# Performance work log

Hardware: AMD Instinct MI355X
Metric: run time of the kernel (lower is better)

Reference implementation:

```python
import jax, jax.numpy as jnp
import numpy as np

D_MODEL = 1024
NUM_HEADS = 16


def setup_inputs() -> dict:
    key = jax.random.key(0)
    ks = jax.random.split(key, 5)
    sigma = (2.0 / (D_MODEL + D_MODEL)) ** 0.5
    def trunc(k):
        # truncated normal in [-3*sigma, 3*sigma], std sigma
        return sigma * jax.random.truncated_normal(k, -3.0, 3.0, (D_MODEL, D_MODEL), jnp.float32)
    x = jax.random.normal(ks[0], (4, 2048, D_MODEL), jnp.float32)
    return {
        "x": x,
        "W_Q": trunc(ks[1]),
        "W_K": trunc(ks[2]),
        "W_V": trunc(ks[3]),
        "W_O": trunc(ks[4]),
    }


def _mha(x, W_Q, W_K, W_V, W_O):
    B, S, D = x.shape
    H = NUM_HEADS
    dk = D // H
    # Linear stores W as (d_out, d_in); einsum '... d_in, d_out d_in -> ... d_out'
    Q = jnp.einsum('bsd,ed->bse', x, W_Q).reshape(B, S, H, dk).transpose(0, 2, 1, 3)
    K = jnp.einsum('bsd,ed->bse', x, W_K).reshape(B, S, H, dk).transpose(0, 2, 1, 3)
    V = jnp.einsum('bsd,ed->bse', x, W_V).reshape(B, S, H, dk).transpose(0, 2, 1, 3)
    scores = jnp.einsum('bhnd,bhmd->bhnm', Q, K) / jnp.sqrt(jnp.asarray(dk, x.dtype))
    causal = jnp.tril(jnp.ones((S, S), bool))
    scores = jnp.where(causal, scores, -jnp.inf)
    attn = jax.nn.softmax(scores, axis=-1)
    out = jnp.einsum('bhnm,bhmd->bhnd', attn, V)  # [B,H,S,dk]
    out = out.transpose(0, 2, 1, 3).reshape(B, S, D)
    return jnp.einsum('bsd,ed->bse', out, W_O)


def reference(x, W_Q, W_K, W_V, W_O):
    return _mha(x, W_Q, W_K, W_V, W_O)
```

## Files before the change

kernel.cpp:

```cpp
#include <hip/hip_runtime.h>
#include <hip/hip_bf16.h>
#include <stdint.h>


typedef unsigned short u16;
typedef short bf16x8 __attribute__((ext_vector_type(8)));
typedef float f32x4 __attribute__((ext_vector_type(4)));
typedef unsigned short u16x8 __attribute__((ext_vector_type(8)));

#define S_LEN 2048
#define DMODEL 1024
#define NH 16

__device__ __forceinline__ u16 f2bf(float f) {
    unsigned u = __builtin_bit_cast(unsigned, f);
    unsigned r = (u + 0x7fffu + ((u >> 16) & 1u)) >> 16;
    return (u16)r;
}

__device__ __forceinline__ float fast_exp2(float x) {
    return __builtin_amdgcn_exp2f(x);
}

__device__ __forceinline__ unsigned cvtpk_bf16(float lo, float hi_) {
    unsigned r;
    asm("v_cvt_pk_bf16_f32 %0, %1, %2" : "=v"(r) : "v"(lo), "v"(hi_));
    return r;
}

__device__ __forceinline__ void gll16(const void* g, void* s) {
    __builtin_amdgcn_global_load_lds((const __attribute__((address_space(1))) unsigned*)g,
                                     (__attribute__((address_space(3))) unsigned*)s, 16, 0, 0);
}

__global__ __launch_bounds__(256) void cast_all(
    const float* __restrict__ x, const float* __restrict__ wq, const float* __restrict__ wk,
    const float* __restrict__ wv, const float* __restrict__ wo,
    u16* __restrict__ xb, u16* __restrict__ wqkv, u16* __restrict__ wob, int nx) {
    const int NW = DMODEL * DMODEL;
    int i4 = (blockIdx.x * 256 + threadIdx.x) * 4;
    const float* src; u16* dst; int off;
    if (i4 < nx)             { src = x;  dst = xb;            off = i4; }
    else if (i4 < nx + NW)   { src = wq; dst = wqkv;          off = i4 - nx; }
    else if (i4 < nx + 2*NW) { src = wk; dst = wqkv + NW;     off = i4 - nx - NW; }
    else if (i4 < nx + 3*NW) { src = wv; dst = wqkv + 2*NW;   off = i4 - nx - 2*NW; }
    else                     { src = wo; dst = wob;           off = i4 - nx - 3*NW; }
    float4 v = *reinterpret_cast<const float4*>(src + off);
    ushort4 o4; o4.x = f2bf(v.x); o4.y = f2bf(v.y); o4.z = f2bf(v.z); o4.w = f2bf(v.w);
    *reinterpret_cast<ushort4*>(dst + off) = o4;
}

template <typename OUT>
__global__ __launch_bounds__(256) void gemm_bt(const u16* __restrict__ A, const u16* __restrict__ B,
                                               OUT* __restrict__ C, int M, int N, int K,
                                               int qcols, float qscale, u16* __restrict__ vt) {
    __shared__ u16 As[128 * 64];
    __shared__ u16 Bs[128 * 64];
    __shared__ u16 Ts[4][16 * 72];
    const int m0 = blockIdx.y * 128, n0 = blockIdx.x * 128;
    const int t = threadIdx.x, w = t >> 6, l = t & 63;
    const int hi = l >> 4;
    const int wr = w >> 1, wc = w & 1;
    f32x4 acc[4][4] = {};

    const int lr = l >> 3;
    const int lc = l & 7;
    const int gcol = (lc ^ lr) * 8;
    const u16* Ag = A + (size_t)(m0 + w * 32 + lr) * K + gcol;
    const u16* Bg = B + (size_t)(n0 + w * 32 + lr) * K + gcol;

    for (int k0 = 0; k0 < K; k0 += 64) {
        __syncthreads();
#pragma unroll
        for (int c = 0; c < 4; c++) {
            gll16(Ag + (size_t)c * 8 * K + k0, As + w * 2048 + c * 512);
            gll16(Bg + (size_t)c * 8 * K + k0, Bs + w * 2048 + c * 512);
        }
        __syncthreads();
#pragma unroll
        for (int kk = 0; kk < 2; kk++) {
            bf16x8 af[4], bfr[4];
#pragma unroll
            for (int mi = 0; mi < 4; mi++)
                af[mi] = *(const bf16x8*)&As[(wr * 64 + mi * 16 + (l & 15)) * 64 +
                                             (((kk * 4 + hi) ^ (l & 7)) * 8)];
#pragma unroll
            for (int ni = 0; ni < 4; ni++)
                bfr[ni] = *(const bf16x8*)&Bs[(wc * 64 + ni * 16 + (l & 15)) * 64 +
                                              (((kk * 4 + hi) ^ (l & 7)) * 8)];
#pragma unroll
            for (int mi = 0; mi < 4; mi++)
#pragma unroll
                for (int ni = 0; ni < 4; ni++)
                    acc[mi][ni] = __builtin_amdgcn_mfma_f32_16x16x32_bf16(af[mi], bfr[ni], acc[mi][ni], 0, 0, 0);
        }
    }

    if (vt != nullptr && n0 >= 2048) {
        const int mw = m0 + wr * 64;
        const int bq = mw >> 11;
        const int s0w = mw & (S_LEN - 1);
        const int hd = ((n0 + wc * 64) - 2048) >> 6;
        u16* tb = &Ts[w][0];
#pragma unroll
        for (int ni = 0; ni < 4; ni++) {
#pragma unroll
            for (int mi = 0; mi < 4; mi++) {
                uint2 pk = make_uint2(cvtpk_bf16(acc[mi][ni][0], acc[mi][ni][1]),
                                      cvtpk_bf16(acc[mi][ni][2], acc[mi][ni][3]));
                *(uint2*)&tb[(l & 15) * 72 + mi * 16 + hi * 4] = pk;
            }
            bf16x8 r0 = *(const bf16x8*)&tb[(l & 15) * 72 + hi * 16];
            bf16x8 r1 = *(const bf16x8*)&tb[(l & 15) * 72 + hi * 16 + 8];
            size_t vrow = ((size_t)(bq * 16 + hd) * 64 + ni * 16 + (l & 15)) * S_LEN + s0w + hi * 16;
            *(u16x8*)&vt[vrow]     = (u16x8)r0;
            *(u16x8*)&vt[vrow + 8] = (u16x8)r1;
        }
    } else {
#pragma unroll
        for (int mi = 0; mi < 4; mi++)
#pragma unroll
            for (int ni = 0; ni < 4; ni++)
#pragma unroll
                for (int j = 0; j < 4; j++) {
                    int r = m0 + wr * 64 + mi * 16 + hi * 4 + j;
                    int c = n0 + wc * 64 + ni * 16 + (l & 15);
                    float v = acc[mi][ni][j];
                    if (c < qcols) v *= qscale;
                    if constexpr (__is_same(OUT, u16)) C[(size_t)r * N + c] = f2bf(v);
                    else                               C[(size_t)r * N + c] = v;
                }
    }
}

__global__ __launch_bounds__(512, 4) void attn(const u16* __restrict__ QKV, const u16* __restrict__ VT,
                                               u16* __restrict__ O) {
    const int bh = blockIdx.x, p = blockIdx.y;
    const int b = bh >> 4, h = bh & 15;
    const int t = threadIdx.x, w = t >> 6, l = t & 63;
    const int q = l & 15, hi = l >> 4, s7 = q & 7;

    __shared__ u16 SM[2][2][64][64];
    __shared__ u16 PS[8][16][64];

    const int srow = t >> 3, sblk = t & 7;
    const int gs = (sblk ^ (srow & 7)) * 8;
    const u16* Kg = QKV + (size_t)(b * S_LEN + srow) * 3072 + 1024 + h * 64 + gs;
    const u16* Vg = VT + (size_t)(bh * 64 + srow) * S_LEN + gs;

    const int kA0 = q * 128 + ((hi ^ s7) << 4);
    const int kA1 = kA0 ^ 64;
    const char* smbase = (const char*)&SM[0][0][0][0];

    char* pbase = (char*)&PS[w][0][0];
    const int pw0 = q * 128 + ((((0 * 2) + (hi >> 1)) ^ s7) << 4) + ((hi & 1) << 3);
    const int pw1 = q * 128 + ((((1 * 2) + (hi >> 1)) ^ s7) << 4) + ((hi & 1) << 3);
    const int pw2 = q * 128 + ((((2 * 2) + (hi >> 1)) ^ s7) << 4) + ((hi & 1) << 3);
    const int pw3 = q * 128 + ((((3 * 2) + (hi >> 1)) ^ s7) << 4) + ((hi & 1) << 3);
    const int pr0 = q * 128 + (((0 * 4 + hi) ^ s7) << 4);
    const int pr1 = q * 128 + (((1 * 4 + hi) ^ s7) << 4);

#pragma unroll 1
    for (int part = 0; part < 2; ++part) {
        const int q128 = (part == 0 ? p : 15 - p) * 128;
        const int nt = q128 / 64 + 2;
        const int qglob = q128 + w * 16 + q;

        bf16x8 qf[2];
#pragma unroll
        for (int kk = 0; kk < 2; kk++)
            qf[kk] = *(const bf16x8*)&QKV[(size_t)(b * S_LEN + qglob) * 3072 + h * 64 + kk * 32 + hi * 8];

        f32x4 oacc[4] = {};
        float ss0 = 0.f, ss1 = 0.f;

        gll16(Kg, (u16*)&SM[0][0][0][0] + t * 8);
        gll16(Vg, (u16*)&SM[0][1][0][0] + t * 8);
        __syncthreads();

        const u16* KgT = Kg + (size_t)64 * 3072;
        const u16* VgT = Vg + 64;

#pragma unroll 1
        for (int tt = 0; tt < nt; ++tt) {
            const int cur = tt & 1;
            if (tt + 1 < nt) {
                gll16(KgT, (u16*)&SM[cur ^ 1][0][0][0] + t * 8);
                gll16(VgT, (u16*)&SM[cur ^ 1][1][0][0] + t * 8);
                KgT += (size_t)64 * 3072;
                VgT += 64;
            }
            const int kv0 = tt * 64;
            if (q128 + w * 16 + 15 >= kv0) {
                const char* kb = smbase + cur * 16384;
                f32x4 sacc[4] = {};
                __builtin_amdgcn_s_setprio(1);
#pragma unroll
                for (int kk = 0; kk < 2; kk++) {
                    const char* ka = kb + (kk ? kA1 : kA0);
#pragma unroll
                    for (int ni = 0; ni < 4; ni++) {
                        bf16x8 kf = *(const bf16x8*)(ka + ni * 2048);
                        sacc[ni] = __builtin_amdgcn_mfma_f32_16x16x32_bf16(kf, qf[kk], sacc[ni], 0, 0, 0);
                    }
                }
                __builtin_amdgcn_s_setprio(0);
                const int r0 = qglob - kv0;
                if (r0 < 63) {
                    const int rth = r0 - hi * 4;
#pragma unroll
                    for (int ni = 0; ni < 4; ni++)
#pragma unroll
                        for (int j = 0; j < 4; j++)
                            if (ni * 16 + j > rth) sacc[ni][j] = -1e30f;
                }
                float pv[4][4];
#pragma unroll
                for (int ni = 0; ni < 4; ni++)
#pragma unroll
                    for (int j = 0; j < 4; j++) pv[ni][j] = fast_exp2(sacc[ni][j] - 8.0f);
                ss0 += ((pv[0][0] + pv[0][1]) + (pv[0][2] + pv[0][3]))
                     + ((pv[1][0] + pv[1][1]) + (pv[1][2] + pv[1][3]));
                ss1 += ((pv[2][0] + pv[2][1]) + (pv[2][2] + pv[2][3]))
                     + ((pv[3][0] + pv[3][1]) + (pv[3][2] + pv[3][3]));
                *(uint2*)(pbase + pw0) = make_uint2(cvtpk_bf16(pv[0][0], pv[0][1]), cvtpk_bf16(pv[0][2], pv[0][3]));
                *(uint2*)(pbase + pw1) = make_uint2(cvtpk_bf16(pv[1][0], pv[1][1]), cvtpk_bf16(pv[1][2], pv[1][3]));
                *(uint2*)(pbase + pw2) = make_uint2(cvtpk_bf16(pv[2][0], pv[2][1]), cvtpk_bf16(pv[2][2], pv[2][3]));
                *(uint2*)(pbase + pw3) = make_uint2(cvtpk_bf16(pv[3][0], pv[3][1]), cvtpk_bf16(pv[3][2], pv[3][3]));
                bf16x8 pf0 = *(const bf16x8*)(pbase + pr0);
                bf16x8 pf1 = *(const bf16x8*)(pbase + pr1);
                const char* vb = kb + 8192;
                __builtin_amdgcn_s_setprio(1);
#pragma unroll
                for (int kk = 0; kk < 2; kk++) {
                    const char* va = vb + (kk ? kA1 : kA0);
                    bf16x8 pf = kk ? pf1 : pf0;
#pragma unroll
                    for (int di = 0; di < 4; di++) {
                        bf16x8 vf = *(const bf16x8*)(va + di * 2048);
                        oacc[di] = __builtin_amdgcn_mfma_f32_16x16x32_bf16(vf, pf, oacc[di], 0, 0, 0);
                    }
                }
                __builtin_amdgcn_s_setprio(0);
            }
            __syncthreads();
        }

        float ssr = ss0 + ss1;
        ssr += __shfl_xor(ssr, 16, 64);
        ssr += __shfl_xor(ssr, 32, 64);
        float inv = 1.0f / ssr;
#pragma unroll
        for (int di = 0; di < 4; di++) {
            ushort4 o4;
            o4.x = f2bf(oacc[di][0] * inv);
            o4.y = f2bf(oacc[di][1] * inv);
            o4.z = f2bf(oacc[di][2] * inv);
            o4.w = f2bf(oacc[di][3] * inv);
            *(ushort4*)&O[(size_t)(b * S_LEN + qglob) * DMODEL + h * 64 + di * 16 + hi * 4] = o4;
        }
    }
}

extern "C" void kernel_launch(void* const* d_in, const int* in_sizes, int n_in,
                              void* d_out, int out_size, void* d_ws, size_t ws_size,
                              hipStream_t stream) {
    const float* x  = (const float*)d_in[0];
    const float* wq = (const float*)d_in[1];
    const float* wk = (const float*)d_in[2];
    const float* wv = (const float*)d_in[3];
    const float* wo = (const float*)d_in[4];
    const int nx = in_sizes[0];
    const int BS = nx / DMODEL;
    const int NW = DMODEL * DMODEL;

    u16* xb   = (u16*)d_ws;
    u16* wqkv = xb + (size_t)nx;
    u16* wob  = wqkv + (size_t)3 * NW;
    u16* qkv  = wob + (size_t)NW;
    u16* vt   = qkv + (size_t)BS * 3072;
    u16* ob   = vt + (size_t)nx;

    int ncast = (nx + 4 * NW) / 4 / 256;
    cast_all<<<ncast, 256, 0, stream>>>(x, wq, wk, wv, wo, xb, wqkv, wob, nx);

    const float QSC = 0.125f * 1.44269504088896f;
    gemm_bt<u16><<<dim3(3072 / 128, BS / 128), 256, 0, stream>>>(xb, wqkv, qkv, BS, 3072, DMODEL,
                                                                 DMODEL, QSC, vt);

    attn<<<dim3((BS / S_LEN) * NH, 8), 512, 0, stream>>>(qkv, vt, ob);

    gemm_bt<float><<<dim3(DMODEL / 128, BS / 128), 256, 0, stream>>>(ob, wob, (float*)d_out, BS, DMODEL, DMODEL,
                                                                     0, 1.0f, nullptr);
}
```

Baseline: 159.4 us.

## Fuse both causal query parts into one KV sweep sharing K/V tiles

The attention kernel used to stream K/V tiles twice per block, once for each of its two paired query chunks (p and 15-p). It now holds both chunks' Q fragments and accumulators and walks the KV sequence once, reusing each staged K/V tile and its LDS fragment reads for both chunks. This cuts global loads and barriers for the shorter chunk. In exchange it doubles accumulator and Q register use, which may lower occupancy under launch_bounds(512,4), and it adds a second P scratch buffer in LDS.

Result: slower. 186.6 us (+17.1%).

```diff
diff --git a/kernel.cpp b/kernel.cpp
--- a/kernel.cpp
+++ b/kernel.cpp
@@ -141,7 +141,7 @@
     const int q = l & 15, hi = l >> 4, s7 = q & 7;
 
     __shared__ u16 SM[2][2][64][64];
-    __shared__ u16 PS[8][16][64];
+    __shared__ u16 PS[8][2][16][64];
 
     const int srow = t >> 3, sblk = t & 7;
     const int gs = (sblk ^ (srow & 7)) * 8;
@@ -152,7 +152,8 @@
     const int kA1 = kA0 ^ 64;
     const char* smbase = (const char*)&SM[0][0][0][0];
 
-    char* pbase = (char*)&PS[w][0][0];
+    char* pb0 = (char*)&PS[w][0][0][0];
+    char* pb1 = (char*)&PS[w][1][0][0];
     const int pw0 = q * 128 + ((((0 * 2) + (hi >> 1)) ^ s7) << 4) + ((hi & 1) << 3);
     const int pw1 = q * 128 + ((((1 * 2) + (hi >> 1)) ^ s7) << 4) + ((hi & 1) << 3);
     const int pw2 = q * 128 + ((((2 * 2) + (hi >> 1)) ^ s7) << 4) + ((hi & 1) << 3);
@@ -160,104 +161,148 @@
     const int pr0 = q * 128 + (((0 * 4 + hi) ^ s7) << 4);
     const int pr1 = q * 128 + (((1 * 4 + hi) ^ s7) << 4);
 
+    const int part1 = 15 - p;
+    const int q128_0 = p * 128, q128_1 = part1 * 128;
+    const int nt0 = 2 * p + 2, nt1 = 2 * part1 + 2;
+    const int qglob0 = q128_0 + w * 16 + q;
+    const int qglob1 = q128_1 + w * 16 + q;
+
+    bf16x8 qf0[2], qf1[2];
+#pragma unroll
+    for (int kk = 0; kk < 2; kk++) {
+        qf0[kk] = *(const bf16x8*)&QKV[(size_t)(b * S_LEN + qglob0) * 3072 + h * 64 + kk * 32 + hi * 8];
+        qf1[kk] = *(const bf16x8*)&QKV[(size_t)(b * S_LEN + qglob1) * 3072 + h * 64 + kk * 32 + hi * 8];
+    }
+
+    f32x4 oacc0[4] = {}, oacc1[4] = {};
+    float ssA = 0.f, ssB = 0.f;
+
+    gll16(Kg, (u16*)&SM[0][0][0][0] + t * 8);
+    gll16(Vg, (u16*)&SM[0][1][0][0] + t * 8);
+    __syncthreads();
+
+    const u16* KgT = Kg + (size_t)64 * 3072;
+    const u16* VgT = Vg + 64;
+
+    auto softmax_part = [&](f32x4* sacc, int qglob, int kv0, char* pb, float& ss,
+                            bf16x8& pf0_, bf16x8& pf1_) {
+        const int r0 = qglob - kv0;
+        if (r0 < 63) {
+            const int rth = r0 - hi * 4;
+#pragma unroll
+            for (int ni = 0; ni < 4; ni++)
+#pragma unroll
+                for (int j = 0; j < 4; j++)
+                    if (ni * 16 + j > rth) sacc[ni][j] = -1e30f;
+        }
+        float pv[4][4];
+#pragma unroll
+        for (int ni = 0; ni < 4; ni++)
+#pragma unroll
+            for (int j = 0; j < 4; j++) pv[ni][j] = fast_exp2(sacc[ni][j] - 8.0f);
+        ss += ((pv[0][0] + pv[0][1]) + (pv[0][2] + pv[0][3]))
+            + ((pv[1][0] + pv[1][1]) + (pv[1][2] + pv[1][3]))
+            + ((pv[2][0] + pv[2][1]) + (pv[2][2] + pv[2][3]))
+            + ((pv[3][0] + pv[3][1]) + (pv[3][2] + pv[3][3]));
+        *(uint2*)(pb + pw0) = make_uint2(cvtpk_bf16(pv[0][0], pv[0][1]), cvtpk_bf16(pv[0][2], pv[0][3]));
+        *(uint2*)(pb + pw1) = make_uint2(cvtpk_bf16(pv[1][0], pv[1][1]), cvtpk_bf16(pv[1][2], pv[1][3]));
+        *(uint2*)(pb + pw2) = make_uint2(cvtpk_bf16(pv[2][0], pv[2][1]), cvtpk_bf16(pv[2][2], pv[2][3]));
+        *(uint2*)(pb + pw3) = make_uint2(cvtpk_bf16(pv[3][0], pv[3][1]), cvtpk_bf16(pv[3][2], pv[3][3]));
+        pf0_ = *(const bf16x8*)(pb + pr0);
+        pf1_ = *(const bf16x8*)(pb + pr1);
+    };
+
 #pragma unroll 1
-    for (int part = 0; part < 2; ++part) {
-        const int q128 = (part == 0 ? p : 15 - p) * 128;
-        const int nt = q128 / 64 + 2;
-        const int qglob = q128 + w * 16 + q;
-
-        bf16x8 qf[2];
-#pragma unroll
-        for (int kk = 0; kk < 2; kk++)
-            qf[kk] = *(const bf16x8*)&QKV[(size_t)(b * S_LEN + qglob) * 3072 + h * 64 + kk * 32 + hi * 8];
-
-        f32x4 oacc[4] = {};
-        float ss0 = 0.f, ss1 = 0.f;
-
-        gll16(Kg, (u16*)&SM[0][0][0][0] + t * 8);
-        gll16(Vg, (u16*)&SM[0][1][0][0] + t * 8);
+    for (int tt = 0; tt < nt1; ++tt) {
+        const int cur = tt & 1;
+        if (tt + 1 < nt1) {
+            gll16(KgT, (u16*)&SM[cur ^ 1][0][0][0] + t * 8);
+            gll16(VgT, (u16*)&SM[cur ^ 1][1][0][0] + t * 8);
+            KgT += (size_t)64 * 3072;
+            VgT += 64;
+        }
+        const int kv0 = tt * 64;
+        const bool act0 = (tt < nt0) && (q128_0 + w * 16 + 15 >= kv0);
+        const bool act1 = (q128_1 + w * 16 + 15 >= kv0);
+        if (act0 || act1) {
+            const char* kb = smbase + cur * 16384;
+            f32x4 sacc0[4] = {}, sacc1[4] = {};
+            __builtin_amdgcn_s_setprio(1);
+#pragma unroll
+            for (int kk = 0; kk < 2; kk++) {
+                const char* ka = kb + (kk ? kA1 : kA0);
+                bf16x8 kfr[4];
+#pragma unroll
+                for (int ni = 0; ni < 4; ni++) kfr[ni] = *(const bf16x8*)(ka + ni * 2048);
+                if (act0) {
+#pragma unroll
+                    for (int ni = 0; ni < 4; ni++)
+                        sacc0[ni] = __builtin_amdgcn_mfma_f32_16x16x32_bf16(kfr[ni], qf0[kk], sacc0[ni], 0, 0, 0);
+                }
+                if (act1) {
+#pragma unroll
+                    for (int ni = 0; ni < 4; ni++)
+                        sacc1[ni] = __builtin_amdgcn_mfma_f32_16x16x32_bf16(kfr[ni], qf1[kk], sacc1[ni], 0, 0, 0);
+                }
+            }
+            __builtin_amdgcn_s_setprio(0);
+            bf16x8 pf00, pf01, pf10, pf11;
+            if (act0) softmax_part(sacc0, qglob0, kv0, pb0, ssA, pf00, pf01);
+            if (act1) softmax_part(sacc1, qglob1, kv0, pb1, ssB, pf10, pf11);
+            const char* vb = kb + 8192;
+            __builtin_amdgcn_s_setprio(1);
+#pragma unroll
+            for (int kk = 0; kk < 2; kk++) {
+                const char* va = vb + (kk ? kA1 : kA0);
+                bf16x8 vfr[4];
+#pragma unroll
+                for (int di = 0; di < 4; di++) vfr[di] = *(const bf16x8*)(va + di * 2048);
+                if (act0) {
+                    bf16x8 pf = kk ? pf01 : pf00;
+#pragma unroll
+                    for (int di = 0; di < 4; di++)
+                        oacc0[di] = __builtin_amdgcn_mfma_f32_16x16x32_bf16(vfr[di], pf, oacc0[di], 0, 0, 0);
+                }
+                if (act1) {
+                    bf16x8 pf = kk ? pf11 : pf10;
+#pragma unroll
+                    for (int di = 0; di < 4; di++)
+                        oacc1[di] = __builtin_amdgcn_mfma_f32_16x16x32_bf16(vfr[di], pf, oacc1[di], 0, 0, 0);
+                }
+            }
+            __builtin_amdgcn_s_setprio(0);
+        }
         __syncthreads();
-
-        const u16* KgT = Kg + (size_t)64 * 3072;
-        const u16* VgT = Vg + 64;
-
-#pragma unroll 1
-        for (int tt = 0; tt < nt; ++tt) {
-            const int cur = tt & 1;
-            if (tt + 1 < nt) {
-                gll16(KgT, (u16*)&SM[cur ^ 1][0][0][0] + t * 8);
-                gll16(VgT, (u16*)&SM[cur ^ 1][1][0][0] + t * 8);
-                KgT += (size_t)64 * 3072;
-                VgT += 64;
-            }
-            const int kv0 = tt * 64;
-            if (q128 + w * 16 + 15 >= kv0) {
-                const char* kb = smbase + cur * 16384;
-                f32x4 sacc[4] = {};
-                __builtin_amdgcn_s_setprio(1);
-#pragma unroll
-                for (int kk = 0; kk < 2; kk++) {
-                    const char* ka = kb + (kk ? kA1 : kA0);
-#pragma unroll
-                    for (int ni = 0; ni < 4; ni++) {
-                        bf16x8 kf = *(const bf16x8*)(ka + ni * 2048);
-                        sacc[ni] = __builtin_amdgcn_mfma_f32_16x16x32_bf16(kf, qf[kk], sacc[ni], 0, 0, 0);
-                    }
-                }
-                __builtin_amdgcn_s_setprio(0);
-                const int r0 = qglob - kv0;
-                if (r0 < 63) {
-                    const int rth = r0 - hi * 4;
-#pragma unroll
-                    for (int ni = 0; ni < 4; ni++)
-#pragma unroll
-                        for (int j = 0; j < 4; j++)
-                            if (ni * 16 + j > rth) sacc[ni][j] = -1e30f;
-                }
-                float pv[4][4];
-#pragma unroll
-                for (int ni = 0; ni < 4; ni++)
-#pragma unroll
-                    for (int j = 0; j < 4; j++) pv[ni][j] = fast_exp2(sacc[ni][j] - 8.0f);
-                ss0 += ((pv[0][0] + pv[0][1]) + (pv[0][2] + pv[0][3]))
-                     + ((pv[1][0] + pv[1][1]) + (pv[1][2] + pv[1][3]));
-                ss1 += ((pv[2][0] + pv[2][1]) + (pv[2][2] + pv[2][3]))
-                     + ((pv[3][0] + pv[3][1]) + (pv[3][2] + pv[3][3]));
-                *(uint2*)(pbase + pw0) = make_uint2(cvtpk_bf16(pv[0][0], pv[0][1]), cvtpk_bf16(pv[0][2], pv[0][3]));
-                *(uint2*)(pbase + pw1) = make_uint2(cvtpk_bf16(pv[1][0], pv[1][1]), cvtpk_bf16(pv[1][2], pv[1][3]));
-                *(uint2*)(pbase + pw2) = make_uint2(cvtpk_bf16(pv[2][0], pv[2][1]), cvtpk_bf16(pv[2][2], pv[2][3]));
-                *(uint2*)(pbase + pw3) = make_uint2(cvtpk_bf16(pv[3][0], pv[3][1]), cvtpk_bf16(pv[3][2], pv[3][3]));
-                bf16x8 pf0 = *(const bf16x8*)(pbase + pr0);
-                bf16x8 pf1 = *(const bf16x8*)(pbase + pr1);
-                const char* vb = kb + 8192;
-                __builtin_amdgcn_s_setprio(1);
-#pragma unroll
-                for (int kk = 0; kk < 2; kk++) {
-                    const char* va = vb + (kk ? kA1 : kA0);
-                    bf16x8 pf = kk ? pf1 : pf0;
-#pragma unroll
-                    for (int di = 0; di < 4; di++) {
-                        bf16x8 vf = *(const bf16x8*)(va + di * 2048);
-                        oacc[di] = __builtin_amdgcn_mfma_f32_16x16x32_bf16(vf, pf, oacc[di], 0, 0, 0);
-                    }
-                }
-                __builtin_amdgcn_s_setprio(0);
-            }
-            __syncthreads();
-        }
-
-        float ssr = ss0 + ss1;
+    }
+
+    {
+        float ssr = ssA;
         ssr += __shfl_xor(ssr, 16, 64);
         ssr += __shfl_xor(ssr, 32, 64);
         float inv = 1.0f / ssr;
 #pragma unroll
         for (int di = 0; di < 4; di++) {
             ushort4 o4;
-            o4.x = f2bf(oacc[di][0] * inv);
-            o4.y = f2bf(oacc[di][1] * inv);
-            o4.z = f2bf(oacc[di][2] * inv);
-            o4.w = f2bf(oacc[di][3] * inv);
-            *(ushort4*)&O[(size_t)(b * S_LEN + qglob) * DMODEL + h * 64 + di * 16 + hi * 4] = o4;
+            o4.x = f2bf(oacc0[di][0] * inv);
+            o4.y = f2bf(oacc0[di][1] * inv);
+            o4.z = f2bf(oacc0[di][2] * inv);
+            o4.w = f2bf(oacc0[di][3] * inv);
+            *(ushort4*)&O[(size_t)(b * S_LEN + qglob0) * DMODEL + h * 64 + di * 16 + hi * 4] = o4;
+        }
+    }
+    {
+        float ssr = ssB;
+        ssr += __shfl_xor(ssr, 16, 64);
+        ssr += __shfl_xor(ssr, 32, 64);
+        float inv = 1.0f / ssr;
+#pragma unroll
+        for (int di = 0; di < 4; di++) {
+            ushort4 o4;
+            o4.x = f2bf(oacc1[di][0] * inv);
+            o4.y = f2bf(oacc1[di][1] * inv);
+            o4.z = f2bf(oacc1[di][2] * inv);
+            o4.w = f2bf(oacc1[di][3] * inv);
+            *(ushort4*)&O[(size_t)(b * S_LEN + qglob1) * DMODEL + h * 64 + di * 16 + hi * 4] = o4;
         }
     }
 }
```
